# Kernel tuning notes

Measured on AMD Instinct MI355X. Metric: run time of the kernel, lower is better.

Reference implementation:

```python
import jax, jax.numpy as jnp
import numpy as np

N_OP, N_TASK, N_TENSOR, N_LINK = 4096, 64, 32768, 1024
N_PLACE = N_OP * N_TASK
NODE_H, EDGE_H = 64, 8
RAW_OP, RAW_TASK, RAW_E = 256, 64, 16
ETYPES = ['link', 'prev', 'succ', 'place', 'serve']
N_LAYERS = 6


def setup_inputs():
    key = jax.random.key(0)
    ks = jax.random.split(key, 20)
    f = jnp.float32
    def w(k, shape, fan_in):
        return jax.random.normal(k, shape, f) / np.sqrt(fan_in)
    return {
        'op_feats': jax.random.normal(ks[0], (N_OP, RAW_OP), f),
        'task_feats': jax.random.normal(ks[1], (N_TASK, RAW_TASK), f),
        'tensor_feats': jax.random.normal(ks[2], (N_TENSOR, RAW_E), f),
        'link_feats': jax.random.normal(ks[3], (N_LINK, RAW_E), f),
        'place_feats': jax.random.normal(ks[4], (N_PLACE, RAW_E), f),
        'prev_src': jax.random.randint(ks[5], (N_TENSOR,), 0, N_OP, jnp.int32),
        'prev_dst': jax.random.randint(ks[6], (N_TENSOR,), 0, N_OP, jnp.int32),
        'link_src': jax.random.randint(ks[7], (N_LINK,), 0, N_TASK, jnp.int32),
        'link_dst': jax.random.randint(ks[8], (N_LINK,), 0, N_TASK, jnp.int32),
        'op_W': w(ks[9], (RAW_OP, NODE_H), RAW_OP),
        'op_b': jnp.zeros((NODE_H,), f),
        'task_W': w(ks[10], (RAW_TASK, NODE_H), RAW_TASK),
        'task_b': jnp.zeros((NODE_H,), f),
        # 5 per-etype edge-trans Dense layers, all raw edge dim = RAW_E
        'eW': w(ks[11], (5, RAW_E, EDGE_H), RAW_E),
        'eb': jnp.zeros((5, EDGE_H), f),
        # GConv Dense per (etype, layer): input = NODE_H + EDGE_H = 72
        'gW': w(ks[12], (5, N_LAYERS, NODE_H + EDGE_H, NODE_H), NODE_H + EDGE_H),
        'gb': jnp.zeros((5, N_LAYERS, NODE_H), f),
        'final_W': w(ks[13], (NODE_H + EDGE_H + NODE_H, 1), NODE_H + EDGE_H + NODE_H),
        'final_b': jnp.zeros((1,), f),
    }


def _mean_agg(msgs, dst, num_segments):
    s = jax.ops.segment_sum(msgs, dst, num_segments=num_segments)
    cnt = jax.ops.segment_sum(jnp.ones((msgs.shape[0], 1), msgs.dtype), dst,
                              num_segments=num_segments)
    return s / jnp.maximum(cnt, 1.0)


def _forward(op_feats, task_feats, tensor_feats, link_feats, place_feats,
             op_W, op_b, task_W, task_b, eW, eb, gW, gb, final_W, final_b,
             prev_src, prev_dst, link_src, link_dst):
    elu = jax.nn.elu
    op = elu(op_feats @ op_W + op_b)      # [N_OP, 64]
    task = elu(task_feats @ task_W + task_b)  # [N_TASK, 64]

    raw_e = {'link': link_feats, 'prev': tensor_feats, 'succ': tensor_feats,
             'place': place_feats, 'serve': place_feats}
    ef = {et: elu(raw_e[et] @ eW[i] + eb[i]) for i, et in enumerate(ETYPES)}

    # place edges: complete bipartite, row-major by op (matches final reshape)
    place_src = jnp.repeat(jnp.arange(N_OP, dtype=jnp.int32), N_TASK)
    place_dst = jnp.tile(jnp.arange(N_TASK, dtype=jnp.int32), N_OP)

    # etype -> (src_idx, dst_idx, src_kind, dst_kind)
    topo = {
        'link':  (link_src, link_dst, 'task', 'task'),
        'prev':  (prev_src, prev_dst, 'op', 'op'),
        'succ':  (prev_dst, prev_src, 'op', 'op'),
        'place': (place_src, place_dst, 'op', 'task'),
        'serve': (place_dst, place_src, 'task', 'op'),
    }
    n_nodes = {'op': N_OP, 'task': N_TASK}

    for l in range(N_LAYERS):
        op_dst, task_dst = [], []
        for i, et in enumerate(ETYPES):
            sidx, didx, skind, dkind = topo[et]
            src = op if skind == 'op' else task
            # gather-concat-Dense per edge: [E, 72] @ [72, 64]
            m = jnp.concatenate([src[sidx], ef[et]], axis=1) @ gW[i, l] + gb[i, l]
            o = _mean_agg(m, didx, n_nodes[dkind])
            (op_dst if dkind == 'op' else task_dst).append(o)
        op = elu(op + sum(op_dst) / len(op_dst))
        task = elu(task + sum(task_dst) / len(task_dst))

    # final per-place-edge score: concat(src op, place edge feat, dst task)
    d = jnp.concatenate([op[place_src], ef['place'], task[place_dst]], axis=1)
    d = d @ final_W + final_b  # [N_PLACE, 1]
    return jnp.reshape(d[:, 0], (N_OP, N_TASK))


def reference(op_feats, task_feats, tensor_feats, link_feats, place_feats,
              prev_src, prev_dst, link_src, link_dst,
              op_W, op_b, task_W, task_b, eW, eb, gW, gb, final_W, final_b):
    return _forward(op_feats, task_feats, tensor_feats, link_feats, place_feats,
                    op_W, op_b, task_W, task_b, eW, eb, gW, gb, final_W, final_b,
                    prev_src, prev_dst, link_src, link_dst)
```

## Files before the change

### kernel.cpp

```cpp
#include <hip/hip_runtime.h>
#include <math.h>

#define NOP 4096
#define NTASK 64
#define NTENSOR 32768
#define NLINK 1024
#define NPLACE (NOP*NTASK)
#define CAP 64
#define NOPB 512

enum : int {
  O_CNT_PREV  = 0,
  O_CNT_SUCC  = O_CNT_PREV + NOP,
  O_CNT_LINK  = O_CNT_SUCC + NOP,
  O_SEF_PREV  = O_CNT_LINK + 64,
  O_SEF_SUCC  = O_SEF_PREV + NOP*8,
  O_SEF_LINK  = O_SEF_SUCC + NOP*8,
  O_SEF_PLACE = O_SEF_LINK + 64*8,
  O_SEF_SERVE = O_SEF_PLACE + 64*8,
  O_OP_A      = O_SEF_SERVE + NOP*8,
  O_OP_B      = O_OP_A + NOP*64,
  O_TASK_A    = O_OP_B + NOP*64,
  O_TASK_B    = O_TASK_A + 64*64,
  O_BPLACE    = O_TASK_B + 64*64,
  O_AOP       = O_BPLACE + NPLACE,
  O_CVEC      = O_AOP + NOP,
  O_MOPP      = O_CVEC + 64,
  O_MTPP      = O_MOPP + 2*512*64,
  O_SPLP      = O_MTPP + 2*4*64,
  O_CSRP_PREV = O_SPLP + 256*512,
  O_CSRP_SUCC = O_CSRP_PREV + NOP*CAP,
  O_CSRP_LINK = O_CSRP_SUCC + NOP*CAP,
  O_EFS_PREV  = O_CSRP_LINK + 64*CAP,
  O_EFS_SUCC  = O_EFS_PREV + NOP*CAP*8,
  O_EFS_LINK  = O_EFS_SUCC + NOP*CAP*8,
  O_TOTAL     = O_EFS_LINK + 64*CAP*8
};

__device__ __forceinline__ float elu1(float x) { return x > 0.f ? x : expm1f(x); }

__device__ __forceinline__ void fma4(float4& a, const float s, const float4 w) {
  a.x = fmaf(s, w.x, a.x);
  a.y = fmaf(s, w.y, a.y);
  a.z = fmaf(s, w.z, a.z);
  a.w = fmaf(s, w.w, a.w);
}

__global__ __launch_bounds__(256) void k_embed(
    const float* __restrict__ opA, const float* __restrict__ opW, const float* __restrict__ opb,
    const float* __restrict__ taskA, const float* __restrict__ taskW, const float* __restrict__ taskb,
    float* __restrict__ ws)
{
  __shared__ float smem[9280];
  const int tid = threadIdx.x;
  const int bid = blockIdx.x;
  if (bid < 256) {
    float* sW = smem;
    float* sA = smem + 4096;
    float4* red = (float4*)(smem + 8256);
    const int obase = bid * 16;
    for (int i = tid; i < 4096; i += 256) {
      const int o = i >> 8, k = i & 255;
      sA[o*260 + k] = opA[(size_t)(obase + o)*256 + k];
    }
    const int o = tid >> 4, hq = tid & 15, h0 = hq*4;
    float4 acc = *(const float4*)&opb[h0];
    for (int q = 0; q < 4; ++q) {
      __syncthreads();
      for (int i = tid*4; i < 4096; i += 1024)
        *(float4*)&sW[i] = *(const float4*)&opW[q*4096 + i];
      __syncthreads();
      const float* a = &sA[o*260 + q*64];
      for (int k = 0; k < 64; ++k)
        fma4(acc, a[k], *(const float4*)&sW[k*64 + h0]);
    }
    acc.x = elu1(acc.x); acc.y = elu1(acc.y); acc.z = elu1(acc.z); acc.w = elu1(acc.w);
    *(float4*)&ws[O_OP_A + (size_t)(obase + o)*64 + h0] = acc;
    red[tid] = acc;
    __syncthreads();
    if (tid < 16) {
      float4 s = make_float4(0.f,0.f,0.f,0.f);
      for (int g = 0; g < 16; ++g) {
        float4 v = red[g*16 + tid];
        s.x += v.x; s.y += v.y; s.z += v.z; s.w += v.w;
      }
      *(float4*)&ws[O_MOPP + bid*64 + tid*4] = s;
    }
  } else {
    float* sA = smem;
    float* sW = smem + 4160;
    float4* red = (float4*)(smem + 8256);
    int* ib = (int*)ws;
    for (int i = tid; i < NOP*2 + 64; i += 256) ib[O_CNT_PREV + i] = 0;
    for (int i = tid; i < 4096; i += 256) {
      const int t = i >> 6, k = i & 63;
      sA[t*65 + k] = taskA[i];
    }
    for (int i = tid*4; i < 4096; i += 1024)
      *(float4*)&sW[i] = *(const float4*)&taskW[i];
    __syncthreads();
    const int og = tid >> 4, hq = tid & 15, h0 = hq*4;
    float4 msum = make_float4(0.f,0.f,0.f,0.f);
    for (int tg = 0; tg < 4; ++tg) {
      const int t = tg*16 + og;
      float4 acc = *(const float4*)&taskb[h0];
      const float* a = &sA[t*65];
      for (int k = 0; k < 64; ++k)
        fma4(acc, a[k], *(const float4*)&sW[k*64 + h0]);
      acc.x = elu1(acc.x); acc.y = elu1(acc.y); acc.z = elu1(acc.z); acc.w = elu1(acc.w);
      *(float4*)&ws[O_TASK_A + t*64 + h0] = acc;
      msum.x += acc.x; msum.y += acc.y; msum.z += acc.z; msum.w += acc.w;
    }
    red[tid] = msum;
    __syncthreads();
    if (tid < 16) {
      float4 s = make_float4(0.f,0.f,0.f,0.f);
      for (int g = 0; g < 16; ++g) {
        float4 v = red[g*16 + tid];
        s.x += v.x; s.y += v.y; s.z += v.z; s.w += v.w;
      }
      *(float4*)&ws[O_MTPP + tid*4] = s;
    }
  }
}

__global__ __launch_bounds__(256) void k_edge_place(
    const float* __restrict__ tensor_feats, const float* __restrict__ link_feats,
    const float* __restrict__ place_feats,
    const int* __restrict__ prev_src, const int* __restrict__ prev_dst,
    const int* __restrict__ link_src, const int* __restrict__ link_dst,
    const float* __restrict__ eW, const float* __restrict__ eb,
    const float* __restrict__ finalW, float* __restrict__ ws)
{
  __shared__ float smem[792];
  const int tid = threadIdx.x;
  const int bid = blockIdx.x;
  int* ib = (int*)ws;
  if (bid < 128) {
    float* sEW = smem;
    float* sEB = smem + 384;
    for (int i = tid; i < 384; i += 256) sEW[i] = eW[i];
    if (tid < 24) sEB[tid] = eb[tid];
    __syncthreads();
    const int e = bid*256 + tid;
    float raw[16];
    *(float4*)&raw[0]  = *(const float4*)&tensor_feats[(size_t)e*16 + 0];
    *(float4*)&raw[4]  = *(const float4*)&tensor_feats[(size_t)e*16 + 4];
    *(float4*)&raw[8]  = *(const float4*)&tensor_feats[(size_t)e*16 + 8];
    *(float4*)&raw[12] = *(const float4*)&tensor_feats[(size_t)e*16 + 12];
    float efp[8], efs[8];
#pragma unroll
    for (int c = 0; c < 8; ++c) { efp[c] = sEB[8+c]; efs[c] = sEB[16+c]; }
#pragma unroll
    for (int k = 0; k < 16; ++k) {
      const float a = raw[k];
#pragma unroll
      for (int c = 0; c < 8; ++c) {
        efp[c] = fmaf(a, sEW[128 + k*8 + c], efp[c]);
        efs[c] = fmaf(a, sEW[256 + k*8 + c], efs[c]);
      }
    }
#pragma unroll
    for (int c = 0; c < 8; ++c) { efp[c] = elu1(efp[c]); efs[c] = elu1(efs[c]); }
    const int pd = prev_dst[e], ps = prev_src[e];
    {
      int pos = atomicAdd(&ib[O_CNT_PREV + pd], 1);
      if (pos < CAP) {
        ib[O_CSRP_PREV + pd*CAP + pos] = ps;
        float* dst = ws + O_EFS_PREV + ((size_t)pd*CAP + pos)*8;
        *(float4*)&dst[0] = make_float4(efp[0],efp[1],efp[2],efp[3]);
        *(float4*)&dst[4] = make_float4(efp[4],efp[5],efp[6],efp[7]);
      }
    }
    {
      int pos = atomicAdd(&ib[O_CNT_SUCC + ps], 1);
      if (pos < CAP) {
        ib[O_CSRP_SUCC + ps*CAP + pos] = pd;
        float* dst = ws + O_EFS_SUCC + ((size_t)ps*CAP + pos)*8;
        *(float4*)&dst[0] = make_float4(efs[0],efs[1],efs[2],efs[3]);
        *(float4*)&dst[4] = make_float4(efs[4],efs[5],efs[6],efs[7]);
      }
    }
    if (e < NLINK) {
      float rl[16];
      *(float4*)&rl[0]  = *(const float4*)&link_feats[(size_t)e*16 + 0];
      *(float4*)&rl[4]  = *(const float4*)&link_feats[(size_t)e*16 + 4];
      *(float4*)&rl[8]  = *(const float4*)&link_feats[(size_t)e*16 + 8];
      *(float4*)&rl[12] = *(const float4*)&link_feats[(size_t)e*16 + 12];
      float efl[8];
#pragma unroll
      for (int c = 0; c < 8; ++c) efl[c] = sEB[c];
#pragma unroll
      for (int k = 0; k < 16; ++k) {
        const float a = rl[k];
#pragma unroll
        for (int c = 0; c < 8; ++c) efl[c] = fmaf(a, sEW[k*8 + c], efl[c]);
      }
      const int ld = link_dst[e];
      int pos = atomicAdd(&ib[O_CNT_LINK + ld], 1);
      if (pos < CAP) {
        ib[O_CSRP_LINK + ld*CAP + pos] = link_src[e];
        float* dst = ws + O_EFS_LINK + ((size_t)ld*CAP + pos)*8;
        *(float4*)&dst[0] = make_float4(elu1(efl[0]),elu1(efl[1]),elu1(efl[2]),elu1(efl[3]));
        *(float4*)&dst[4] = make_float4(elu1(efl[4]),elu1(efl[5]),elu1(efl[6]),elu1(efl[7]));
      }
    }
  } else {
    float* sW3 = smem;
    float* sW4 = smem + 128;
    float* sB3 = smem + 256;
    float* sB4 = smem + 264;
    float* sW1 = smem + 272;
    float* pl  = smem + 280;
    const int pbid = bid - 128;
    if (tid < 128) { sW3[tid] = eW[3*128 + tid]; sW4[tid] = eW[4*128 + tid]; }
    if (tid < 8) { sB3[tid] = eb[24+tid]; sB4[tid] = eb[32+tid]; sW1[tid] = finalW[64+tid]; }
    for (int i = tid; i < 512; i += 256) pl[i] = 0.f;
    __syncthreads();
    const int lane = tid & 63;
    const int wave = (pbid*256 + tid) >> 6;
    float pacc[8];
#pragma unroll
    for (int c = 0; c < 8; ++c) pacc[c] = 0.f;
    float* bplace = ws + O_BPLACE;
    float* sserve = ws + O_SEF_SERVE;
    for (int j = 0; j < 4; ++j) {
      const int i = wave*4 + j;
      const int e = i*64 + lane;
      float raw[16];
      *(float4*)&raw[0]  = *(const float4*)&place_feats[(size_t)e*16 + 0];
      *(float4*)&raw[4]  = *(const float4*)&place_feats[(size_t)e*16 + 4];
      *(float4*)&raw[8]  = *(const float4*)&place_feats[(size_t)e*16 + 8];
      *(float4*)&raw[12] = *(const float4*)&place_feats[(size_t)e*16 + 12];
      float efp[8], efs[8];
#pragma unroll
      for (int c = 0; c < 8; ++c) { efp[c] = sB3[c]; efs[c] = sB4[c]; }
#pragma unroll
      for (int k = 0; k < 16; ++k) {
        const float a = raw[k];
#pragma unroll
        for (int c = 0; c < 8; ++c) {
          efp[c] = fmaf(a, sW3[k*8 + c], efp[c]);
          efs[c] = fmaf(a, sW4[k*8 + c], efs[c]);
        }
      }
      float bp = 0.f;
#pragma unroll
      for (int c = 0; c < 8; ++c) {
        efp[c] = elu1(efp[c]);
        efs[c] = elu1(efs[c]);
        bp = fmaf(efp[c], sW1[c], bp);
        pacc[c] += efp[c];
      }
      bplace[e] = bp;
#pragma unroll
      for (int c = 0; c < 8; ++c) {
        float v = efs[c];
        for (int m = 32; m >= 1; m >>= 1) v += __shfl_xor(v, m, 64);
        if (lane == 0) sserve[i*8 + c] = v;
      }
    }
#pragma unroll
    for (int c = 0; c < 8; ++c) atomicAdd(&pl[lane*8 + c], pacc[c]);
    __syncthreads();
    for (int i = tid; i < 512; i += 256) ws[O_SPLP + pbid*512 + i] = pl[i];
  }
}

__global__ __launch_bounds__(256) void k_layer(
    const int l,
    const float* __restrict__ gW, const float* __restrict__ gb,
    const float* __restrict__ finalW,
    const float* __restrict__ op_in, float* __restrict__ op_out,
    const float* __restrict__ task_in, float* __restrict__ task_out,
    float* __restrict__ ws)
{
  __shared__ float smem[12544];
  const int tid = threadIdx.x;
  const int bid = blockIdx.x;
  const int* ib = (const int*)ws;
  const int rpar = l & 1, wpar = 1 - rpar;

  if (bid < NOPB) {
    float* sWp    = smem;
    float* sWs    = smem + 4608;
    float* sWeS   = smem + 9216;
    float* vp     = smem + 9728;
    float* sums_p = smem + 9984;
    float* sums_s = smem + 10528;
    float* sGB    = smem + 11072;
    float* sef    = smem + 11200;
    float* mop    = smem + 11392;
    int* idxp_s   = (int*)(smem + 11456);
    int* idxs_s   = (int*)(smem + 11968);
    int* cp_s     = (int*)(smem + 12480);
    int* cs_s     = (int*)(smem + 12488);

    const int obase = bid*8;
    const float* gWprev  = gW + (size_t)((6  + l)*72)*64;
    const float* gWsucc  = gW + (size_t)((12 + l)*72)*64;
    const float* gWserve = gW + (size_t)((24 + l)*72)*64;

    for (int i = tid*4; i < 4608; i += 1024) {
      *(float4*)&sWp[i] = *(const float4*)&gWprev[i];
      *(float4*)&sWs[i] = *(const float4*)&gWsucc[i];
    }
    if (tid*4 < 512) *(float4*)&sWeS[tid*4] = *(const float4*)&gWserve[4096 + tid*4];
    if (tid < 8) cp_s[tid] = ib[O_CNT_PREV + obase + tid];
    else if (tid < 16) cs_s[tid-8] = ib[O_CNT_SUCC + obase + (tid-8)];
    for (int i = tid; i < 8*CAP; i += 256) {
      const int o = i >> 6, j = i & 63;
      if (j < ib[O_CNT_PREV + obase + o]) idxp_s[i] = ib[O_CSRP_PREV + (obase+o)*CAP + j];
      if (j < ib[O_CNT_SUCC + obase + o]) idxs_s[i] = ib[O_CSRP_SUCC + (obase+o)*CAP + j];
    }
    if (tid < 128) sGB[tid] = (tid < 64) ? gb[(6+l)*64 + tid] : gb[(12+l)*64 + (tid-64)];
    if (tid < 64) mop[tid] = 0.f;
    if (l == 0) {
      if (tid >= 128 && tid < 192) sef[tid] = ws[O_SEF_SERVE + obase*8 + (tid-128)];
    } else {
      if (tid < 64)       sef[tid] = ws[O_SEF_PREV + obase*8 + tid];
      else if (tid < 128) sef[tid] = ws[O_SEF_SUCC + obase*8 + (tid-64)];
      else if (tid < 192) sef[tid] = ws[O_SEF_SERVE + obase*8 + (tid-128)];
    }
    {
      const int col = tid & 63, g = tid >> 6;
      const float* mtpp = ws + O_MTPP + rpar*256;
      const int nst = (l == 0) ? 1 : 4;
      float acc = (g == 0) ? gb[(24+l)*64 + col] : 0.f;
      for (int kk = 0; kk < 16; ++kk) {
        const int k = g*16 + kk;
        float mt = 0.f;
        for (int s = 0; s < nst; ++s) mt += mtpp[s*64 + k];
        acc = fmaf(mt*(1.f/64.f), gWserve[k*64 + col], acc);
      }
      vp[g*64 + col] = acc;
    }
    __syncthreads();

    const int wv = tid >> 6, lane = tid & 63;
#pragma unroll
    for (int oo = 0; oo < 2; ++oo) {
      const int o = 2*wv + oo;
      const int pep = min(cp_s[o], CAP);
      const int pes = min(cs_s[o], CAP);
      const int* ip = &idxp_s[o*CAP];
      const int* iq = &idxs_s[o*CAP];
      float p0=0.f,p1=0.f,p2=0.f,p3=0.f,q0=0.f,q1=0.f,q2=0.f,q3=0.f;
      int p = 0, q = 0;
      while (p+3 < pep && q+3 < pes) {
        const int a0=ip[p],a1=ip[p+1],a2=ip[p+2],a3=ip[p+3];
        const int b0=iq[q],b1=iq[q+1],b2=iq[q+2],b3=iq[q+3];
        p0 += op_in[(size_t)a0*64 + lane];
        p1 += op_in[(size_t)a1*64 + lane];
        p2 += op_in[(size_t)a2*64 + lane];
        p3 += op_in[(size_t)a3*64 + lane];
        q0 += op_in[(size_t)b0*64 + lane];
        q1 += op_in[(size_t)b1*64 + lane];
        q2 += op_in[(size_t)b2*64 + lane];
        q3 += op_in[(size_t)b3*64 + lane];
        p += 4; q += 4;
      }
      for (; p+3 < pep; p += 4) {
        const int a0=ip[p],a1=ip[p+1],a2=ip[p+2],a3=ip[p+3];
        p0 += op_in[(size_t)a0*64 + lane];
        p1 += op_in[(size_t)a1*64 + lane];
        p2 += op_in[(size_t)a2*64 + lane];
        p3 += op_in[(size_t)a3*64 + lane];
      }
      for (; q+3 < pes; q += 4) {
        const int b0=iq[q],b1=iq[q+1],b2=iq[q+2],b3=iq[q+3];
        q0 += op_in[(size_t)b0*64 + lane];
        q1 += op_in[(size_t)b1*64 + lane];
        q2 += op_in[(size_t)b2*64 + lane];
        q3 += op_in[(size_t)b3*64 + lane];
      }
      for (; p < pep; ++p) p0 += op_in[(size_t)ip[p]*64 + lane];
      for (; q < pes; ++q) q0 += op_in[(size_t)iq[q]*64 + lane];
      sums_p[o*68 + lane] = (p0+p1)+(p2+p3);
      sums_s[o*68 + lane] = (q0+q1)+(q2+q3);
    }
    if (l == 0) {
      if (tid < 128) {
        const bool isP = (tid < 64);
        const int t2 = tid & 63;
        const int o = t2 >> 3, c = t2 & 7;
        const int cnt = min(isP ? cp_s[o] : cs_s[o], CAP);
        const float* efs = ws + (isP ? O_EFS_PREV : O_EFS_SUCC) + ((size_t)(obase+o)*CAP)*8;
        float s0=0.f,s1=0.f,s2=0.f,s3=0.f;
        int j = 0;
        for (; j+3 < cnt; j += 4) {
          s0 += efs[j*8+c]; s1 += efs[(j+1)*8+c];
          s2 += efs[(j+2)*8+c]; s3 += efs[(j+3)*8+c];
        }
        for (; j < cnt; ++j) s0 += efs[j*8+c];
        const float s = (s0+s1)+(s2+s3);
        sef[tid] = s;
        ws[(isP ? O_SEF_PREV : O_SEF_SUCC) + obase*8 + t2] = s;
      }
    }
    __syncthreads();

    const int oL = tid >> 5, c = (tid & 31)*2;
    const int d  = obase + oL;
    float up0 = 0.f, up1 = 0.f, us0 = 0.f, us1 = 0.f;
    const int cp = cp_s[oL];
    if (cp > 0) {
      float a0 = 0.f, a1 = 0.f;
      for (int k = 0; k < 64; ++k) {
        const float sk = sums_p[oL*68 + k];
        const float2 wv2 = *(const float2*)&sWp[k*64 + c];
        a0 = fmaf(sk, wv2.x, a0);
        a1 = fmaf(sk, wv2.y, a1);
      }
#pragma unroll
      for (int cc = 0; cc < 8; ++cc) {
        const float ev = sef[oL*8 + cc];
        const float2 wv2 = *(const float2*)&sWp[4096 + cc*64 + c];
        a0 = fmaf(ev, wv2.x, a0);
        a1 = fmaf(ev, wv2.y, a1);
      }
      const float r = 1.f/(float)cp;
      up0 = fmaf(a0, r, sGB[c]);
      up1 = fmaf(a1, r, sGB[c+1]);
    }
    const int cs = cs_s[oL];
    if (cs > 0) {
      float a0 = 0.f, a1 = 0.f;
      for (int k = 0; k < 64; ++k) {
        const float sk = sums_s[oL*68 + k];
        const float2 wv2 = *(const float2*)&sWs[k*64 + c];
        a0 = fmaf(sk, wv2.x, a0);
        a1 = fmaf(sk, wv2.y, a1);
      }
#pragma unroll
      for (int cc = 0; cc < 8; ++cc) {
        const float ev = sef[64 + oL*8 + cc];
        const float2 wv2 = *(const float2*)&sWs[4096 + cc*64 + c];
        a0 = fmaf(ev, wv2.x, a0);
        a1 = fmaf(ev, wv2.y, a1);
      }
      const float r = 1.f/(float)cs;
      us0 = fmaf(a0, r, sGB[64 + c]);
      us1 = fmaf(a1, r, sGB[64 + c + 1]);
    }
    float g0, g1;
    {
      const float2 v0 = *(const float2*)&vp[c];
      const float2 v1 = *(const float2*)&vp[64 + c];
      const float2 v2 = *(const float2*)&vp[128 + c];
      const float2 v3 = *(const float2*)&vp[192 + c];
      g0 = (v0.x + v1.x) + (v2.x + v3.x);
      g1 = (v0.y + v1.y) + (v2.y + v3.y);
#pragma unroll
      for (int cc = 0; cc < 8; ++cc) {
        const float ev = sef[128 + oL*8 + cc] * (1.f/64.f);
        const float2 wv2 = *(const float2*)&sWeS[cc*64 + c];
        g0 = fmaf(ev, wv2.x, g0);
        g1 = fmaf(ev, wv2.y, g1);
      }
    }
    const float2 x = *(const float2*)&op_in[(size_t)d*64 + c];
    const float r0 = elu1(x.x + (up0 + us0 + g0)*(1.f/3.f));
    const float r1 = elu1(x.y + (up1 + us1 + g1)*(1.f/3.f));
    if (l < 5) {
      float2 xo; xo.x = r0; xo.y = r1;
      *(float2*)&op_out[(size_t)d*64 + c] = xo;
      atomicAdd(&mop[c],   r0);
      atomicAdd(&mop[c+1], r1);
      __syncthreads();
      if (tid < 64) ws[O_MOPP + wpar*32768 + bid*64 + tid] = mop[tid];
    } else {
      float av = r0*finalW[c] + r1*finalW[c+1];
      av += __shfl_xor(av, 1, 64);
      av += __shfl_xor(av, 2, 64);
      av += __shfl_xor(av, 4, 64);
      av += __shfl_xor(av, 8, 64);
      av += __shfl_xor(av, 16, 64);
      if ((tid & 31) == 0) ws[O_AOP + d] = av;
    }
  } else {
    const int tbase = (bid - NOPB)*16;
    float* sTask  = smem;
    float* sW0    = smem + 4096;
    float* sWe3   = smem + 8704;
    float* vpl    = smem + 9216;
    float* mo4    = smem + 9472;
    float* sums_l = smem + 9728;
    float* sGB0   = smem + 10816;
    float* sefl   = smem + 10880;
    float* sefpl  = smem + 11008;
    float* mtp    = smem + 11136;
    int* idxl_s   = (int*)(smem + 11200);
    int* cl_s     = (int*)(smem + 12224);

    const float* gWlink  = gW + (size_t)(l*72)*64;
    const float* gWplace = gW + (size_t)((18 + l)*72)*64;

    {
      const int col = tid & 63, g = tid >> 6;
      const float* mopp = ws + O_MOPP + rpar*32768;
      const int nso = (l == 0) ? 256 : 512;
      float a0=0.f,a1=0.f,a2=0.f,a3=0.f,a4=0.f,a5=0.f,a6=0.f,a7=0.f;
      for (int s = g; s < nso; s += 32) {
        a0 += mopp[(s+0 )*64 + col];
        a1 += mopp[(s+4 )*64 + col];
        a2 += mopp[(s+8 )*64 + col];
        a3 += mopp[(s+12)*64 + col];
        a4 += mopp[(s+16)*64 + col];
        a5 += mopp[(s+20)*64 + col];
        a6 += mopp[(s+24)*64 + col];
        a7 += mopp[(s+28)*64 + col];
      }
      mo4[g*64 + col] = ((a0+a1)+(a2+a3)) + ((a4+a5)+(a6+a7));
    }
    for (int i = tid*4; i < 4096; i += 1024)
      *(float4*)&sTask[i] = *(const float4*)&task_in[i];
    for (int i = tid*4; i < 4608; i += 1024)
      *(float4*)&sW0[i] = *(const float4*)&gWlink[i];
    if (tid*4 < 512) *(float4*)&sWe3[tid*4] = *(const float4*)&gWplace[4096 + tid*4];
    if (tid < 16) cl_s[tid] = ib[O_CNT_LINK + tbase + tid];
    for (int i = tid; i < 16*CAP; i += 256) {
      const int t = i >> 6, j = i & 63;
      if (j < ib[O_CNT_LINK + tbase + t]) idxl_s[i] = ib[O_CSRP_LINK + (tbase+t)*CAP + j];
    }
    if (tid < 64) { sGB0[tid] = gb[l*64 + tid]; mtp[tid] = 0.f; }
    if (l == 0) {
      if (tid < 128) {
        const int t = tid >> 3, c = tid & 7;
        const int cnt = min(ib[O_CNT_LINK + tbase + t], CAP);
        const float* efs = ws + O_EFS_LINK + ((size_t)(tbase+t)*CAP)*8;
        float s0 = 0.f, s1 = 0.f;
        int j = 0;
        for (; j+1 < cnt; j += 2) { s0 += efs[j*8+c]; s1 += efs[j*8+8+c]; }
        if (j < cnt) s0 += efs[j*8+c];
        const float s = s0 + s1;
        sefl[tid] = s;
        ws[O_SEF_LINK + tbase*8 + tid] = s;
      } else {
        const int idx = tid - 128;
        float s0=0.f,s1=0.f,s2=0.f,s3=0.f;
        for (int r = 0; r < 256; r += 4) {
          s0 += ws[O_SPLP + (r+0)*512 + tbase*8 + idx];
          s1 += ws[O_SPLP + (r+1)*512 + tbase*8 + idx];
          s2 += ws[O_SPLP + (r+2)*512 + tbase*8 + idx];
          s3 += ws[O_SPLP + (r+3)*512 + tbase*8 + idx];
        }
        const float s = (s0+s1)+(s2+s3);
        sefpl[idx] = s;
        ws[O_SEF_PLACE + tbase*8 + idx] = s;
      }
    } else {
      if (tid < 128) sefl[tid] = ws[O_SEF_LINK + tbase*8 + tid];
      else sefpl[tid - 128] = ws[O_SEF_PLACE + tbase*8 + (tid - 128)];
    }
    __syncthreads();
    {
      const int col = tid & 63, g = tid >> 6;
      float acc = (g == 0) ? gb[(18+l)*64 + col] : 0.f;
      for (int kk = 0; kk < 16; ++kk) {
        const int k = g*16 + kk;
        const float mok = (mo4[k] + mo4[64+k]) + (mo4[128+k] + mo4[192+k]);
        acc = fmaf(mok*(1.f/4096.f), gWplace[k*64 + col], acc);
      }
      vpl[g*64 + col] = acc;
    }
    __syncthreads();

    const int wv = tid >> 6, lane = tid & 63;
#pragma unroll
    for (int tt = 0; tt < 4; ++tt) {
      const int t = 4*wv + tt;
      const int pe = min(cl_s[t], CAP);
      float s0=0.f,s1=0.f,s2=0.f,s3=0.f;
      int p = 0;
      for (; p+3 < pe; p += 4) {
        s0 += sTask[idxl_s[t*CAP+p  ]*64 + lane];
        s1 += sTask[idxl_s[t*CAP+p+1]*64 + lane];
        s2 += sTask[idxl_s[t*CAP+p+2]*64 + lane];
        s3 += sTask[idxl_s[t*CAP+p+3]*64 + lane];
      }
      for (; p < pe; ++p) s0 += sTask[idxl_s[t*CAP+p]*64 + lane];
      sums_l[t*68 + lane] = (s0+s1)+(s2+s3);
    }

    const int tL = tid >> 4, h0 = (tid & 15)*4;
    const int tG = tbase + tL;
    float4 ul = make_float4(0.f,0.f,0.f,0.f);
    const int cl2 = cl_s[tL];
    if (cl2 > 0) {
      float4 a = make_float4(0.f,0.f,0.f,0.f);
      for (int k = 0; k < 64; ++k)
        fma4(a, sums_l[tL*68 + k], *(const float4*)&sW0[k*64 + h0]);
#pragma unroll
      for (int cc = 0; cc < 8; ++cc)
        fma4(a, sefl[tL*8 + cc], *(const float4*)&sW0[4096 + cc*64 + h0]);
      const float r = 1.f/(float)cl2;
      ul.x = fmaf(a.x, r, sGB0[h0+0]);
      ul.y = fmaf(a.y, r, sGB0[h0+1]);
      ul.z = fmaf(a.z, r, sGB0[h0+2]);
      ul.w = fmaf(a.w, r, sGB0[h0+3]);
    }
    float4 uq;
    {
      const float4 v0 = *(const float4*)&vpl[h0];
      const float4 v1 = *(const float4*)&vpl[64 + h0];
      const float4 v2 = *(const float4*)&vpl[128 + h0];
      const float4 v3 = *(const float4*)&vpl[192 + h0];
      uq.x = (v0.x+v1.x)+(v2.x+v3.x);
      uq.y = (v0.y+v1.y)+(v2.y+v3.y);
      uq.z = (v0.z+v1.z)+(v2.z+v3.z);
      uq.w = (v0.w+v1.w)+(v2.w+v3.w);
#pragma unroll
      for (int cc = 0; cc < 8; ++cc)
        fma4(uq, sefpl[tL*8 + cc]*(1.f/4096.f), *(const float4*)&sWe3[cc*64 + h0]);
    }
    float4 x = *(const float4*)&sTask[tG*64 + h0];
    x.x = elu1(x.x + (ul.x + uq.x)*0.5f);
    x.y = elu1(x.y + (ul.y + uq.y)*0.5f);
    x.z = elu1(x.z + (ul.z + uq.z)*0.5f);
    x.w = elu1(x.w + (ul.w + uq.w)*0.5f);
    if (l < 5) {
      *(float4*)&task_out[(size_t)tG*64 + h0] = x;
      atomicAdd(&mtp[h0+0], x.x);
      atomicAdd(&mtp[h0+1], x.y);
      atomicAdd(&mtp[h0+2], x.z);
      atomicAdd(&mtp[h0+3], x.w);
      __syncthreads();
      if (tid < 64) ws[O_MTPP + wpar*256 + (bid - NOPB)*64 + tid] = mtp[tid];
    } else {
      const float4 fw = *(const float4*)&finalW[72 + h0];
      float cv = x.x*fw.x + x.y*fw.y + x.z*fw.z + x.w*fw.w;
      cv += __shfl_xor(cv, 1, 64);
      cv += __shfl_xor(cv, 2, 64);
      cv += __shfl_xor(cv, 4, 64);
      cv += __shfl_xor(cv, 8, 64);
      if ((tid & 15) == 0) ws[O_CVEC + tG] = cv;
    }
  }
}

__global__ __launch_bounds__(256) void k_final(
    const float* __restrict__ ws, const float* __restrict__ finalb,
    float* __restrict__ out)
{
  const int e4 = (blockIdx.x*256 + threadIdx.x)*4;
  const int i = e4 >> 6;
  const int t = e4 & 63;
  const float a = ws[O_AOP + i];
  const float fb = finalb[0];
  const float4 bp = *(const float4*)&ws[O_BPLACE + e4];
  const float4 cv = *(const float4*)&ws[O_CVEC + t];
  float4 o4;
  o4.x = a + bp.x + cv.x + fb;
  o4.y = a + bp.y + cv.y + fb;
  o4.z = a + bp.z + cv.z + fb;
  o4.w = a + bp.w + cv.w + fb;
  *(float4*)&out[e4] = o4;
}

extern "C" void kernel_launch(void* const* d_in, const int* in_sizes, int n_in,
                              void* d_out, int out_size, void* d_ws, size_t ws_size,
                              hipStream_t stream)
{
  (void)in_sizes; (void)n_in; (void)out_size;
  if (ws_size < (size_t)O_TOTAL * sizeof(float)) return;

  const float* op_feats     = (const float*)d_in[0];
  const float* task_feats   = (const float*)d_in[1];
  const float* tensor_feats = (const float*)d_in[2];
  const float* link_feats   = (const float*)d_in[3];
  const float* place_feats  = (const float*)d_in[4];
  const int*   prev_src     = (const int*)d_in[5];
  const int*   prev_dst     = (const int*)d_in[6];
  const int*   link_src     = (const int*)d_in[7];
  const int*   link_dst     = (const int*)d_in[8];
  const float* op_W         = (const float*)d_in[9];
  const float* op_b         = (const float*)d_in[10];
  const float* task_W       = (const float*)d_in[11];
  const float* task_b       = (const float*)d_in[12];
  const float* eW           = (const float*)d_in[13];
  const float* eb           = (const float*)d_in[14];
  const float* gW           = (const float*)d_in[15];
  const float* gb           = (const float*)d_in[16];
  const float* finalW       = (const float*)d_in[17];
  const float* finalb       = (const float*)d_in[18];
  float* w = (float*)d_ws;
  float* out = (float*)d_out;

  k_embed<<<257, 256, 0, stream>>>(op_feats, op_W, op_b, task_feats, task_W, task_b, w);
  k_edge_place<<<384, 256, 0, stream>>>(tensor_feats, link_feats, place_feats,
                                        prev_src, prev_dst, link_src, link_dst,
                                        eW, eb, finalW, w);

  for (int l = 0; l < 6; ++l) {
    const float* oin  = w + ((l & 1) ? O_OP_B : O_OP_A);
    float*       oout = w + ((l & 1) ? O_OP_A : O_OP_B);
    const float* tin  = w + ((l & 1) ? O_TASK_B : O_TASK_A);
    float*       tout = w + ((l & 1) ? O_TASK_A : O_TASK_B);
    k_layer<<<NOPB + 4, 256, 0, stream>>>(l, gW, gb, finalW, oin, oout, tin, tout, w);
  }

  k_final<<<256, 256, 0, stream>>>(w, finalb, out);
}
```

Baseline: 196.6 us.

## Process 16 ops per layer block and move task blocks first

Each op block in the layer kernel now handles 16 op nodes instead of 8, so the grid shrinks from 516 to 260 blocks. The per-block weight loads (two 72x64 matrices) are amortised over twice as many nodes, and the cross-block partial sums that task blocks must reduce are halved. The four task blocks move to the front of the grid, the layer-0 edge-feature sums move earlier, and the dense step uses float4 per thread. In exchange, shared memory per block grows, parallelism drops to about one block per CU, and each wave gathers for four nodes serially.

```diff
diff --git a/kernel.cpp b/kernel.cpp
--- a/kernel.cpp
+++ b/kernel.cpp
@@ -7,7 +7,6 @@
 #define NLINK 1024
 #define NPLACE (NOP*NTASK)
 #define CAP 64
-#define NOPB 512
 
 enum : int {
   O_CNT_PREV  = 0,
@@ -26,7 +25,7 @@
   O_AOP       = O_BPLACE + NPLACE,
   O_CVEC      = O_AOP + NOP,
   O_MOPP      = O_CVEC + 64,
-  O_MTPP      = O_MOPP + 2*512*64,
+  O_MTPP      = O_MOPP + 2*256*64,
   O_SPLP      = O_MTPP + 2*4*64,
   O_CSRP_PREV = O_SPLP + 256*512,
   O_CSRP_SUCC = O_CSRP_PREV + NOP*CAP,
@@ -275,28 +274,28 @@
     const float* __restrict__ task_in, float* __restrict__ task_out,
     float* __restrict__ ws)
 {
-  __shared__ float smem[12544];
+  __shared__ float smem[14816];
   const int tid = threadIdx.x;
   const int bid = blockIdx.x;
   const int* ib = (const int*)ws;
   const int rpar = l & 1, wpar = 1 - rpar;
 
-  if (bid < NOPB) {
+  if (bid >= 4) {
     float* sWp    = smem;
     float* sWs    = smem + 4608;
     float* sWeS   = smem + 9216;
     float* vp     = smem + 9728;
     float* sums_p = smem + 9984;
-    float* sums_s = smem + 10528;
-    float* sGB    = smem + 11072;
-    float* sef    = smem + 11200;
-    float* mop    = smem + 11392;
-    int* idxp_s   = (int*)(smem + 11456);
-    int* idxs_s   = (int*)(smem + 11968);
-    int* cp_s     = (int*)(smem + 12480);
-    int* cs_s     = (int*)(smem + 12488);
-
-    const int obase = bid*8;
+    float* sums_s = smem + 11072;
+    float* sGB    = smem + 12160;
+    float* sef    = smem + 12288;
+    float* mop    = smem + 12672;
+    int* idxp_s   = (int*)(smem + 12736);
+    int* idxs_s   = (int*)(smem + 13760);
+    int* cp_s     = (int*)(smem + 14784);
+    int* cs_s     = (int*)(smem + 14800);
+
+    const int obase = (bid - 4)*16;
     const float* gWprev  = gW + (size_t)((6  + l)*72)*64;
     const float* gWsucc  = gW + (size_t)((12 + l)*72)*64;
     const float* gWserve = gW + (size_t)((24 + l)*72)*64;
@@ -306,9 +305,11 @@
       *(float4*)&sWs[i] = *(const float4*)&gWsucc[i];
     }
     if (tid*4 < 512) *(float4*)&sWeS[tid*4] = *(const float4*)&gWserve[4096 + tid*4];
-    if (tid < 8) cp_s[tid] = ib[O_CNT_PREV + obase + tid];
-    else if (tid < 16) cs_s[tid-8] = ib[O_CNT_SUCC + obase + (tid-8)];
-    for (int i = tid; i < 8*CAP; i += 256) {
+    if (tid < 16) {
+      cp_s[tid] = ib[O_CNT_PREV + obase + tid];
+      cs_s[tid] = ib[O_CNT_SUCC + obase + tid];
+    }
+    for (int i = tid; i < 16*CAP; i += 256) {
       const int o = i >> 6, j = i & 63;
       if (j < ib[O_CNT_PREV + obase + o]) idxp_s[i] = ib[O_CSRP_PREV + (obase+o)*CAP + j];
       if (j < ib[O_CNT_SUCC + obase + o]) idxs_s[i] = ib[O_CSRP_SUCC + (obase+o)*CAP + j];
@@ -316,11 +317,29 @@
     if (tid < 128) sGB[tid] = (tid < 64) ? gb[(6+l)*64 + tid] : gb[(12+l)*64 + (tid-64)];
     if (tid < 64) mop[tid] = 0.f;
     if (l == 0) {
-      if (tid >= 128 && tid < 192) sef[tid] = ws[O_SEF_SERVE + obase*8 + (tid-128)];
+      const bool isP = (tid < 128);
+      const int t2 = tid & 127;
+      const int o = t2 >> 3, c = t2 & 7;
+      const int cnt = min(ib[(isP ? O_CNT_PREV : O_CNT_SUCC) + obase + o], CAP);
+      const float* efs = ws + (isP ? O_EFS_PREV : O_EFS_SUCC) + ((size_t)(obase+o)*CAP)*8;
+      float s0=0.f,s1=0.f,s2=0.f,s3=0.f;
+      int j = 0;
+      for (; j+3 < cnt; j += 4) {
+        s0 += efs[j*8+c]; s1 += efs[(j+1)*8+c];
+        s2 += efs[(j+2)*8+c]; s3 += efs[(j+3)*8+c];
+      }
+      for (; j < cnt; ++j) s0 += efs[j*8+c];
+      const float s = (s0+s1)+(s2+s3);
+      sef[tid] = s;
+      ws[(isP ? O_SEF_PREV : O_SEF_SUCC) + obase*8 + t2] = s;
+      if (tid < 128) sef[256 + tid] = ws[O_SEF_SERVE + obase*8 + tid];
     } else {
-      if (tid < 64)       sef[tid] = ws[O_SEF_PREV + obase*8 + tid];
-      else if (tid < 128) sef[tid] = ws[O_SEF_SUCC + obase*8 + (tid-64)];
-      else if (tid < 192) sef[tid] = ws[O_SEF_SERVE + obase*8 + (tid-128)];
+      if (tid < 128) {
+        sef[tid]       = ws[O_SEF_PREV + obase*8 + tid];
+        sef[128 + tid] = ws[O_SEF_SUCC + obase*8 + tid];
+      } else {
+        sef[256 + (tid & 127)] = ws[O_SEF_SERVE + obase*8 + (tid & 127)];
+      }
     }
     {
       const int col = tid & 63, g = tid >> 6;
@@ -338,9 +357,8 @@
     __syncthreads();
 
     const int wv = tid >> 6, lane = tid & 63;
-#pragma unroll
-    for (int oo = 0; oo < 2; ++oo) {
-      const int o = 2*wv + oo;
+    for (int oo = 0; oo < 4; ++oo) {
+      const int o = wv*4 + oo;
       const int pep = min(cp_s[o], CAP);
       const int pes = min(cs_s[o], CAP);
       const int* ip = &idxp_s[o*CAP];
@@ -379,117 +397,87 @@
       sums_p[o*68 + lane] = (p0+p1)+(p2+p3);
       sums_s[o*68 + lane] = (q0+q1)+(q2+q3);
     }
-    if (l == 0) {
-      if (tid < 128) {
-        const bool isP = (tid < 64);
-        const int t2 = tid & 63;
-        const int o = t2 >> 3, c = t2 & 7;
-        const int cnt = min(isP ? cp_s[o] : cs_s[o], CAP);
-        const float* efs = ws + (isP ? O_EFS_PREV : O_EFS_SUCC) + ((size_t)(obase+o)*CAP)*8;
-        float s0=0.f,s1=0.f,s2=0.f,s3=0.f;
-        int j = 0;
-        for (; j+3 < cnt; j += 4) {
-          s0 += efs[j*8+c]; s1 += efs[(j+1)*8+c];
-          s2 += efs[(j+2)*8+c]; s3 += efs[(j+3)*8+c];
-        }
-        for (; j < cnt; ++j) s0 += efs[j*8+c];
-        const float s = (s0+s1)+(s2+s3);
-        sef[tid] = s;
-        ws[(isP ? O_SEF_PREV : O_SEF_SUCC) + obase*8 + t2] = s;
-      }
-    }
-    __syncthreads();
-
-    const int oL = tid >> 5, c = (tid & 31)*2;
-    const int d  = obase + oL;
-    float up0 = 0.f, up1 = 0.f, us0 = 0.f, us1 = 0.f;
+
+    const int oL = tid >> 4, h0 = (tid & 15)*4;
+    const int d = obase + oL;
+    float4 up = make_float4(0.f,0.f,0.f,0.f);
+    float4 us = make_float4(0.f,0.f,0.f,0.f);
     const int cp = cp_s[oL];
     if (cp > 0) {
-      float a0 = 0.f, a1 = 0.f;
-      for (int k = 0; k < 64; ++k) {
-        const float sk = sums_p[oL*68 + k];
-        const float2 wv2 = *(const float2*)&sWp[k*64 + c];
-        a0 = fmaf(sk, wv2.x, a0);
-        a1 = fmaf(sk, wv2.y, a1);
-      }
-#pragma unroll
-      for (int cc = 0; cc < 8; ++cc) {
-        const float ev = sef[oL*8 + cc];
-        const float2 wv2 = *(const float2*)&sWp[4096 + cc*64 + c];
-        a0 = fmaf(ev, wv2.x, a0);
-        a1 = fmaf(ev, wv2.y, a1);
-      }
+      float4 a = make_float4(0.f,0.f,0.f,0.f);
+      for (int k = 0; k < 64; ++k)
+        fma4(a, sums_p[oL*68 + k], *(const float4*)&sWp[k*64 + h0]);
+#pragma unroll
+      for (int cc = 0; cc < 8; ++cc)
+        fma4(a, sef[oL*8 + cc], *(const float4*)&sWp[4096 + cc*64 + h0]);
       const float r = 1.f/(float)cp;
-      up0 = fmaf(a0, r, sGB[c]);
-      up1 = fmaf(a1, r, sGB[c+1]);
+      up.x = fmaf(a.x, r, sGB[h0+0]);
+      up.y = fmaf(a.y, r, sGB[h0+1]);
+      up.z = fmaf(a.z, r, sGB[h0+2]);
+      up.w = fmaf(a.w, r, sGB[h0+3]);
     }
     const int cs = cs_s[oL];
     if (cs > 0) {
-      float a0 = 0.f, a1 = 0.f;
-      for (int k = 0; k < 64; ++k) {
-        const float sk = sums_s[oL*68 + k];
-        const float2 wv2 = *(const float2*)&sWs[k*64 + c];
-        a0 = fmaf(sk, wv2.x, a0);
-        a1 = fmaf(sk, wv2.y, a1);
-      }
-#pragma unroll
-      for (int cc = 0; cc < 8; ++cc) {
-        const float ev = sef[64 + oL*8 + cc];
-        const float2 wv2 = *(const float2*)&sWs[4096 + cc*64 + c];
-        a0 = fmaf(ev, wv2.x, a0);
-        a1 = fmaf(ev, wv2.y, a1);
-      }
+      float4 a = make_float4(0.f,0.f,0.f,0.f);
+      for (int k = 0; k < 64; ++k)
+        fma4(a, sums_s[oL*68 + k], *(const float4*)&sWs[k*64 + h0]);
+#pragma unroll
+      for (int cc = 0; cc < 8; ++cc)
+        fma4(a, sef[128 + oL*8 + cc], *(const float4*)&sWs[4096 + cc*64 + h0]);
       const float r = 1.f/(float)cs;
-      us0 = fmaf(a0, r, sGB[64 + c]);
-      us1 = fmaf(a1, r, sGB[64 + c + 1]);
-    }
-    float g0, g1;
+      us.x = fmaf(a.x, r, sGB[64 + h0+0]);
+      us.y = fmaf(a.y, r, sGB[64 + h0+1]);
+      us.z = fmaf(a.z, r, sGB[64 + h0+2]);
+      us.w = fmaf(a.w, r, sGB[64 + h0+3]);
+    }
+    float4 ug;
     {
-      const float2 v0 = *(const float2*)&vp[c];
-      const float2 v1 = *(const float2*)&vp[64 + c];
-      const float2 v2 = *(const float2*)&vp[128 + c];
-      const float2 v3 = *(const float2*)&vp[192 + c];
-      g0 = (v0.x + v1.x) + (v2.x + v3.x);
-      g1 = (v0.y + v1.y) + (v2.y + v3.y);
-#pragma unroll
-      for (int cc = 0; cc < 8; ++cc) {
-        const float ev = sef[128 + oL*8 + cc] * (1.f/64.f);
-        const float2 wv2 = *(const float2*)&sWeS[cc*64 + c];
-        g0 = fmaf(ev, wv2.x, g0);
-        g1 = fmaf(ev, wv2.y, g1);
-      }
-    }
-    const float2 x = *(const float2*)&op_in[(size_t)d*64 + c];
-    const float r0 = elu1(x.x + (up0 + us0 + g0)*(1.f/3.f));
-    const float r1 = elu1(x.y + (up1 + us1 + g1)*(1.f/3.f));
+      const float4 v0 = *(const float4*)&vp[h0];
+      const float4 v1 = *(const float4*)&vp[64 + h0];
+      const float4 v2 = *(const float4*)&vp[128 + h0];
+      const float4 v3 = *(const float4*)&vp[192 + h0];
+      ug.x = (v0.x+v1.x)+(v2.x+v3.x);
+      ug.y = (v0.y+v1.y)+(v2.y+v3.y);
+      ug.z = (v0.z+v1.z)+(v2.z+v3.z);
+      ug.w = (v0.w+v1.w)+(v2.w+v3.w);
+#pragma unroll
+      for (int cc = 0; cc < 8; ++cc)
+        fma4(ug, sef[256 + oL*8 + cc]*(1.f/64.f), *(const float4*)&sWeS[cc*64 + h0]);
+    }
+    float4 x = *(const float4*)&op_in[(size_t)d*64 + h0];
+    x.x = elu1(x.x + (up.x + us.x + ug.x)*(1.f/3.f));
+    x.y = elu1(x.y + (up.y + us.y + ug.y)*(1.f/3.f));
+    x.z = elu1(x.z + (up.z + us.z + ug.z)*(1.f/3.f));
+    x.w = elu1(x.w + (up.w + us.w + ug.w)*(1.f/3.f));
     if (l < 5) {
-      float2 xo; xo.x = r0; xo.y = r1;
-      *(float2*)&op_out[(size_t)d*64 + c] = xo;
-      atomicAdd(&mop[c],   r0);
-      atomicAdd(&mop[c+1], r1);
+      *(float4*)&op_out[(size_t)d*64 + h0] = x;
+      atomicAdd(&mop[h0+0], x.x);
+      atomicAdd(&mop[h0+1], x.y);
+      atomicAdd(&mop[h0+2], x.z);
+      atomicAdd(&mop[h0+3], x.w);
       __syncthreads();
-      if (tid < 64) ws[O_MOPP + wpar*32768 + bid*64 + tid] = mop[tid];
+      if (tid < 64) ws[O_MOPP + wpar*16384 + (bid-4)*64 + tid] = mop[tid];
     } else {
-      float av = r0*finalW[c] + r1*finalW[c+1];
+      const float4 fw = *(const float4*)&finalW[h0];
+      float av = x.x*fw.x + x.y*fw.y + x.z*fw.z + x.w*fw.w;
       av += __shfl_xor(av, 1, 64);
       av += __shfl_xor(av, 2, 64);
       av += __shfl_xor(av, 4, 64);
       av += __shfl_xor(av, 8, 64);
-      av += __shfl_xor(av, 16, 64);
-      if ((tid & 31) == 0) ws[O_AOP + d] = av;
+      if ((tid & 15) == 0) ws[O_AOP + d] = av;
     }
   } else {
-    const int tbase = (bid - NOPB)*16;
+    const int tbase = bid*16;
     float* sTask  = smem;
-    float* sW0    = smem + 4096;
-    float* sWe3   = smem + 8704;
-    float* vpl    = smem + 9216;
-    float* mo4    = smem + 9472;
-    float* sums_l = smem + 9728;
-    float* sGB0   = smem + 10816;
-    float* sefl   = smem + 10880;
-    float* sefpl  = smem + 11008;
-    float* mtp    = smem + 11136;
+    float* vpl    = smem + 4096;
+    float* mo4    = smem + 4352;
+    float* sums_l = smem + 4608;
+    float* sGB0   = smem + 5696;
+    float* sefl   = smem + 5760;
+    float* sefpl  = smem + 5888;
+    float* mtp    = smem + 6016;
+    float* sW0    = smem + 6080;
+    float* sWe3   = smem + 10688;
     int* idxl_s   = (int*)(smem + 11200);
     int* cl_s     = (int*)(smem + 12224);
 
@@ -498,10 +486,9 @@
 
     {
       const int col = tid & 63, g = tid >> 6;
-      const float* mopp = ws + O_MOPP + rpar*32768;
-      const int nso = (l == 0) ? 256 : 512;
+      const float* mopp = ws + O_MOPP + rpar*16384;
       float a0=0.f,a1=0.f,a2=0.f,a3=0.f,a4=0.f,a5=0.f,a6=0.f,a7=0.f;
-      for (int s = g; s < nso; s += 32) {
+      for (int s = g; s < 256; s += 32) {
         a0 += mopp[(s+0 )*64 + col];
         a1 += mopp[(s+4 )*64 + col];
         a2 += mopp[(s+8 )*64 + col];
@@ -626,7 +613,7 @@
       atomicAdd(&mtp[h0+2], x.z);
       atomicAdd(&mtp[h0+3], x.w);
       __syncthreads();
-      if (tid < 64) ws[O_MTPP + wpar*256 + (bid - NOPB)*64 + tid] = mtp[tid];
+      if (tid < 64) ws[O_MTPP + wpar*256 + bid*64 + tid] = mtp[tid];
     } else {
       const float4 fw = *(const float4*)&finalW[72 + h0];
       float cv = x.x*fw.x + x.y*fw.y + x.z*fw.z + x.w*fw.w;
@@ -697,7 +684,7 @@
     float*       oout = w + ((l & 1) ? O_OP_A : O_OP_B);
     const float* tin  = w + ((l & 1) ? O_TASK_B : O_TASK_A);
     float*       tout = w + ((l & 1) ? O_TASK_A : O_TASK_B);
-    k_layer<<<NOPB + 4, 256, 0, stream>>>(l, gW, gb, finalW, oin, oout, tin, tout, w);
+    k_layer<<<260, 256, 0, stream>>>(l, gW, gb, finalW, oin, oout, tin, tout, w);
   }
 
   k_final<<<256, 256, 0, stream>>>(w, finalb, out);
```

New measurement: 213.4 us. +8.5%, slower.

## Stage gconv weights through registers to overlap with gather and drop a barrier

Applied to the files above, without the earlier changes.

Each wave now loads the counts and CSR index lists for its own two op nodes into shared memory, so the gather loop can start without a block-wide barrier. The per-layer prev, succ and serve weight tiles are loaded into registers up front and only written to shared memory after the gather, so their global latency overlaps the neighbour-sum loads. The residual op_in load is also hoisted ahead of the gather. The cost is about 40 extra VGPRs per thread for the staged weights, which may lower occupancy.

```diff
diff --git a/kernel.cpp b/kernel.cpp
--- a/kernel.cpp
+++ b/kernel.cpp
@@ -293,34 +293,44 @@
     float* mop    = smem + 11392;
     int* idxp_s   = (int*)(smem + 11456);
     int* idxs_s   = (int*)(smem + 11968);
-    int* cp_s     = (int*)(smem + 12480);
-    int* cs_s     = (int*)(smem + 12488);
 
     const int obase = bid*8;
     const float* gWprev  = gW + (size_t)((6  + l)*72)*64;
     const float* gWsucc  = gW + (size_t)((12 + l)*72)*64;
     const float* gWserve = gW + (size_t)((24 + l)*72)*64;
 
-    for (int i = tid*4; i < 4608; i += 1024) {
-      *(float4*)&sWp[i] = *(const float4*)&gWprev[i];
-      *(float4*)&sWs[i] = *(const float4*)&gWsucc[i];
-    }
-    if (tid*4 < 512) *(float4*)&sWeS[tid*4] = *(const float4*)&gWserve[4096 + tid*4];
-    if (tid < 8) cp_s[tid] = ib[O_CNT_PREV + obase + tid];
-    else if (tid < 16) cs_s[tid-8] = ib[O_CNT_SUCC + obase + (tid-8)];
-    for (int i = tid; i < 8*CAP; i += 256) {
-      const int o = i >> 6, j = i & 63;
-      if (j < ib[O_CNT_PREV + obase + o]) idxp_s[i] = ib[O_CSRP_PREV + (obase+o)*CAP + j];
-      if (j < ib[O_CNT_SUCC + obase + o]) idxs_s[i] = ib[O_CSRP_SUCC + (obase+o)*CAP + j];
-    }
+    const int wv = tid >> 6, lane = tid & 63;
+    const int o0 = 2*wv, o1 = 2*wv + 1;
+
+    const int cp0 = min(ib[O_CNT_PREV + obase + o0], CAP);
+    const int cp1 = min(ib[O_CNT_PREV + obase + o1], CAP);
+    const int cs0 = min(ib[O_CNT_SUCC + obase + o0], CAP);
+    const int cs1 = min(ib[O_CNT_SUCC + obase + o1], CAP);
+    if (lane < cp0) idxp_s[o0*CAP + lane] = ib[O_CSRP_PREV + (obase+o0)*CAP + lane];
+    if (lane < cp1) idxp_s[o1*CAP + lane] = ib[O_CSRP_PREV + (obase+o1)*CAP + lane];
+    if (lane < cs0) idxs_s[o0*CAP + lane] = ib[O_CSRP_SUCC + (obase+o0)*CAP + lane];
+    if (lane < cs1) idxs_s[o1*CAP + lane] = ib[O_CSRP_SUCC + (obase+o1)*CAP + lane];
+
+    float4 wreg[10];
+#pragma unroll
+    for (int j = 0; j < 10; ++j) {
+      const int i = tid*4 + j*1024;
+      if (i < 9728) {
+        const float* src = (i < 4608) ? &gWprev[i]
+                         : (i < 9216) ? &gWsucc[i - 4608]
+                                      : &gWserve[4096 + (i - 9216)];
+        wreg[j] = *(const float4*)src;
+      }
+    }
+
     if (tid < 128) sGB[tid] = (tid < 64) ? gb[(6+l)*64 + tid] : gb[(12+l)*64 + (tid-64)];
     if (tid < 64) mop[tid] = 0.f;
-    if (l == 0) {
-      if (tid >= 128 && tid < 192) sef[tid] = ws[O_SEF_SERVE + obase*8 + (tid-128)];
-    } else {
+    if (l > 0) {
       if (tid < 64)       sef[tid] = ws[O_SEF_PREV + obase*8 + tid];
       else if (tid < 128) sef[tid] = ws[O_SEF_SUCC + obase*8 + (tid-64)];
       else if (tid < 192) sef[tid] = ws[O_SEF_SERVE + obase*8 + (tid-128)];
+    } else {
+      if (tid >= 128 && tid < 192) sef[tid] = ws[O_SEF_SERVE + obase*8 + (tid-128)];
     }
     {
       const int col = tid & 63, g = tid >> 6;
@@ -335,76 +345,85 @@
       }
       vp[g*64 + col] = acc;
     }
-    __syncthreads();
-
-    const int wv = tid >> 6, lane = tid & 63;
-#pragma unroll
-    for (int oo = 0; oo < 2; ++oo) {
-      const int o = 2*wv + oo;
-      const int pep = min(cp_s[o], CAP);
-      const int pes = min(cs_s[o], CAP);
-      const int* ip = &idxp_s[o*CAP];
-      const int* iq = &idxs_s[o*CAP];
-      float p0=0.f,p1=0.f,p2=0.f,p3=0.f,q0=0.f,q1=0.f,q2=0.f,q3=0.f;
-      int p = 0, q = 0;
-      while (p+3 < pep && q+3 < pes) {
-        const int a0=ip[p],a1=ip[p+1],a2=ip[p+2],a3=ip[p+3];
-        const int b0=iq[q],b1=iq[q+1],b2=iq[q+2],b3=iq[q+3];
-        p0 += op_in[(size_t)a0*64 + lane];
-        p1 += op_in[(size_t)a1*64 + lane];
-        p2 += op_in[(size_t)a2*64 + lane];
-        p3 += op_in[(size_t)a3*64 + lane];
-        q0 += op_in[(size_t)b0*64 + lane];
-        q1 += op_in[(size_t)b1*64 + lane];
-        q2 += op_in[(size_t)b2*64 + lane];
-        q3 += op_in[(size_t)b3*64 + lane];
-        p += 4; q += 4;
-      }
-      for (; p+3 < pep; p += 4) {
-        const int a0=ip[p],a1=ip[p+1],a2=ip[p+2],a3=ip[p+3];
-        p0 += op_in[(size_t)a0*64 + lane];
-        p1 += op_in[(size_t)a1*64 + lane];
-        p2 += op_in[(size_t)a2*64 + lane];
-        p3 += op_in[(size_t)a3*64 + lane];
-      }
-      for (; q+3 < pes; q += 4) {
-        const int b0=iq[q],b1=iq[q+1],b2=iq[q+2],b3=iq[q+3];
-        q0 += op_in[(size_t)b0*64 + lane];
-        q1 += op_in[(size_t)b1*64 + lane];
-        q2 += op_in[(size_t)b2*64 + lane];
-        q3 += op_in[(size_t)b3*64 + lane];
-      }
-      for (; p < pep; ++p) p0 += op_in[(size_t)ip[p]*64 + lane];
-      for (; q < pes; ++q) q0 += op_in[(size_t)iq[q]*64 + lane];
-      sums_p[o*68 + lane] = (p0+p1)+(p2+p3);
-      sums_s[o*68 + lane] = (q0+q1)+(q2+q3);
+    const int oL = tid >> 5, c = (tid & 31)*2;
+    const int d  = obase + oL;
+    const float2 xres = *(const float2*)&op_in[(size_t)d*64 + c];
+
+    {
+      const int cpx[2] = {cp0, cp1};
+      const int csx[2] = {cs0, cs1};
+#pragma unroll
+      for (int oo = 0; oo < 2; ++oo) {
+        const int o = 2*wv + oo;
+        const int pep = cpx[oo];
+        const int pes = csx[oo];
+        const int* ip = &idxp_s[o*CAP];
+        const int* iq = &idxs_s[o*CAP];
+        float p0=0.f,p1=0.f,p2=0.f,p3=0.f,q0=0.f,q1=0.f,q2=0.f,q3=0.f;
+        int p = 0, q = 0;
+        while (p+3 < pep && q+3 < pes) {
+          const int a0=ip[p],a1=ip[p+1],a2=ip[p+2],a3=ip[p+3];
+          const int b0=iq[q],b1=iq[q+1],b2=iq[q+2],b3=iq[q+3];
+          p0 += op_in[(size_t)a0*64 + lane];
+          p1 += op_in[(size_t)a1*64 + lane];
+          p2 += op_in[(size_t)a2*64 + lane];
+          p3 += op_in[(size_t)a3*64 + lane];
+          q0 += op_in[(size_t)b0*64 + lane];
+          q1 += op_in[(size_t)b1*64 + lane];
+          q2 += op_in[(size_t)b2*64 + lane];
+          q3 += op_in[(size_t)b3*64 + lane];
+          p += 4; q += 4;
+        }
+        for (; p+3 < pep; p += 4) {
+          const int a0=ip[p],a1=ip[p+1],a2=ip[p+2],a3=ip[p+3];
+          p0 += op_in[(size_t)a0*64 + lane];
+          p1 += op_in[(size_t)a1*64 + lane];
+          p2 += op_in[(size_t)a2*64 + lane];
+          p3 += op_in[(size_t)a3*64 + lane];
+        }
+        for (; q+3 < pes; q += 4) {
+          const int b0=iq[q],b1=iq[q+1],b2=iq[q+2],b3=iq[q+3];
+          q0 += op_in[(size_t)b0*64 + lane];
+          q1 += op_in[(size_t)b1*64 + lane];
+          q2 += op_in[(size_t)b2*64 + lane];
+          q3 += op_in[(size_t)b3*64 + lane];
+        }
+        for (; p < pep; ++p) p0 += op_in[(size_t)ip[p]*64 + lane];
+        for (; q < pes; ++q) q0 += op_in[(size_t)iq[q]*64 + lane];
+        sums_p[o*68 + lane] = (p0+p1)+(p2+p3);
+        sums_s[o*68 + lane] = (q0+q1)+(q2+q3);
+      }
     }
     if (l == 0) {
       if (tid < 128) {
         const bool isP = (tid < 64);
         const int t2 = tid & 63;
-        const int o = t2 >> 3, c = t2 & 7;
-        const int cnt = min(isP ? cp_s[o] : cs_s[o], CAP);
+        const int o = t2 >> 3, cc = t2 & 7;
+        const int cnt = min(ib[(isP ? O_CNT_PREV : O_CNT_SUCC) + obase + o], CAP);
         const float* efs = ws + (isP ? O_EFS_PREV : O_EFS_SUCC) + ((size_t)(obase+o)*CAP)*8;
         float s0=0.f,s1=0.f,s2=0.f,s3=0.f;
         int j = 0;
         for (; j+3 < cnt; j += 4) {
-          s0 += efs[j*8+c]; s1 += efs[(j+1)*8+c];
-          s2 += efs[(j+2)*8+c]; s3 += efs[(j+3)*8+c];
+          s0 += efs[j*8+cc]; s1 += efs[(j+1)*8+cc];
+          s2 += efs[(j+2)*8+cc]; s3 += efs[(j+3)*8+cc];
         }
-        for (; j < cnt; ++j) s0 += efs[j*8+c];
+        for (; j < cnt; ++j) s0 += efs[j*8+cc];
         const float s = (s0+s1)+(s2+s3);
         sef[tid] = s;
         ws[(isP ? O_SEF_PREV : O_SEF_SUCC) + obase*8 + t2] = s;
       }
     }
-    __syncthreads();
-
-    const int oL = tid >> 5, c = (tid & 31)*2;
-    const int d  = obase + oL;
+#pragma unroll
+    for (int j = 0; j < 10; ++j) {
+      const int i = tid*4 + j*1024;
+      if (i < 9728) *(float4*)&smem[i] = wreg[j];
+    }
+    __syncthreads();
+
+    const int cpL = (lane >> 5) ? cp1 : cp0;
+    const int csL = (lane >> 5) ? cs1 : cs0;
     float up0 = 0.f, up1 = 0.f, us0 = 0.f, us1 = 0.f;
-    const int cp = cp_s[oL];
-    if (cp > 0) {
+    if (cpL > 0) {
       float a0 = 0.f, a1 = 0.f;
       for (int k = 0; k < 64; ++k) {
         const float sk = sums_p[oL*68 + k];
@@ -419,12 +438,11 @@
         a0 = fmaf(ev, wv2.x, a0);
         a1 = fmaf(ev, wv2.y, a1);
       }
-      const float r = 1.f/(float)cp;
+      const float r = 1.f/(float)cpL;
       up0 = fmaf(a0, r, sGB[c]);
       up1 = fmaf(a1, r, sGB[c+1]);
     }
-    const int cs = cs_s[oL];
-    if (cs > 0) {
+    if (csL > 0) {
       float a0 = 0.f, a1 = 0.f;
       for (int k = 0; k < 64; ++k) {
         const float sk = sums_s[oL*68 + k];
@@ -439,7 +457,7 @@
         a0 = fmaf(ev, wv2.x, a0);
         a1 = fmaf(ev, wv2.y, a1);
       }
-      const float r = 1.f/(float)cs;
+      const float r = 1.f/(float)csL;
       us0 = fmaf(a0, r, sGB[64 + c]);
       us1 = fmaf(a1, r, sGB[64 + c + 1]);
     }
@@ -459,9 +477,8 @@
         g1 = fmaf(ev, wv2.y, g1);
       }
     }
-    const float2 x = *(const float2*)&op_in[(size_t)d*64 + c];
-    const float r0 = elu1(x.x + (up0 + us0 + g0)*(1.f/3.f));
-    const float r1 = elu1(x.y + (up1 + us1 + g1)*(1.f/3.f));
+    const float r0 = elu1(xres.x + (up0 + us0 + g0)*(1.f/3.f));
+    const float r1 = elu1(xres.y + (up1 + us1 + g1)*(1.f/3.f));
     if (l < 5) {
       float2 xo; xo.x = r0; xo.y = r1;
       *(float2*)&op_out[(size_t)d*64 + c] = xo;
```

Result: slower. 218.2 us (+11.0%).
